# Kernel optimization log

Measured on AMD Instinct MI355X. Metric: run time of the kernel, lower is better.

## Reference

```python
import jax, jax.numpy as jnp
import numpy as np

B, S, D, H = 4, 4096, 2048, 512
EPS = 1e-5


def setup_inputs() -> dict:
    key = jax.random.key(0)
    ks = jax.random.split(key, 5)
    x = jax.random.normal(ks[0], (B, S, D), dtype=jnp.float32)
    ln_gamma = jnp.ones((D,), dtype=jnp.float32)
    ln_beta = jnp.zeros((D,), dtype=jnp.float32)
    # 'small' init: uniform in [1e-5 - 1e-6, 1e-5 + 1e-6]; use scaled randn here
    # so gradients are non-trivial, same math either way.
    W_down = jax.random.normal(ks[1], (H, D), dtype=jnp.float32) * 0.02
    b_down = jax.random.normal(ks[2], (H,), dtype=jnp.float32) * 0.02
    W_up = jax.random.normal(ks[3], (D, H), dtype=jnp.float32) * 0.02
    b_up = jax.random.normal(ks[4], (D,), dtype=jnp.float32) * 0.02
    return {"x": x, "ln_gamma": ln_gamma, "ln_beta": ln_beta,
            "W_down": W_down, "b_down": b_down, "W_up": W_up, "b_up": b_up}


def _layer_norm(x, gamma, beta):
    mu = jnp.mean(x, axis=-1, keepdims=True)
    var = jnp.mean(jnp.square(x - mu), axis=-1, keepdims=True)
    return (x - mu) * jax.lax.rsqrt(var + EPS) * gamma + beta


def reference(x, ln_gamma, ln_beta, W_down, b_down, W_up, b_up):
    # LayerNorm -> down-proj -> ReLU -> up-proj -> residual add
    y = _layer_norm(x, ln_gamma, ln_beta)                      # [B,S,D]
    y = jnp.einsum('bsd,hd->bsh', y, W_down) + b_down          # [B,S,H]
    y = jax.nn.relu(y)
    y = jnp.einsum('bsh,dh->bsd', y, W_up) + b_up              # [B,S,D]
    return x + y
```

## Files before the change

### kernel.cpp

```cpp
#include <hip/hip_runtime.h>

#define DD 2048
#define HH 512
#define NTOK 16384

typedef __attribute__((ext_vector_type(8))) short short8_t;
typedef __attribute__((ext_vector_type(4))) short short4_t;
typedef __attribute__((ext_vector_type(4))) float f32x4;

static __device__ __forceinline__ short f2bf(float f) {
    union { float f; unsigned u; } v; v.f = f;
    unsigned r = (v.u + 0x7fffu + ((v.u >> 16) & 1u)) >> 16;
    return (short)r;
}

static __device__ __forceinline__ void gl16(const short* g, short* l) {
    __builtin_amdgcn_global_load_lds(
        (const __attribute__((address_space(1))) unsigned int*)g,
        (__attribute__((address_space(3))) unsigned int*)l, 16, 0, 0);
}

__global__ __launch_bounds__(256) void k_wprep(
    const float* __restrict__ Wd, const float* __restrict__ g,
    const float* __restrict__ be, const float* __restrict__ Wu,
    short* __restrict__ Wg, short* __restrict__ Wub,
    float* __restrict__ c1, float* __restrict__ c2)
{
    int bid = blockIdx.x;
    if (bid < 128) {
        int w = threadIdx.x >> 6, lane = threadIdx.x & 63;
        int h = bid * 4 + w;
        const float* wr = Wd + (size_t)h * DD;
        float s1 = 0.f, s2 = 0.f;
        for (int i = 0; i < 8; i++) {
            int col = i * 256 + lane * 4;
            float4 wv = *(const float4*)(wr + col);
            float4 gv = *(const float4*)(g + col);
            float4 bv = *(const float4*)(be + col);
            s1 += gv.x * wv.x + gv.y * wv.y + gv.z * wv.z + gv.w * wv.w;
            s2 += bv.x * wv.x + bv.y * wv.y + bv.z * wv.z + bv.w * wv.w;
            short4_t o;
            o[0] = f2bf(wv.x * gv.x); o[1] = f2bf(wv.y * gv.y);
            o[2] = f2bf(wv.z * gv.z); o[3] = f2bf(wv.w * gv.w);
            *(short4_t*)(Wg + (size_t)h * DD + col) = o;
        }
        for (int m = 1; m < 64; m <<= 1) { s1 += __shfl_xor(s1, m); s2 += __shfl_xor(s2, m); }
        if (lane == 0) { c1[h] = s1; c2[h] = s2; }
    } else {
        int b = bid - 128;
        for (int r = 0; r < 4; r++) {
            int i = (b * 4 + r) * 1024 + threadIdx.x * 4;
            float4 v = *(const float4*)(Wu + i);
            short4_t o;
            o[0] = f2bf(v.x); o[1] = f2bf(v.y); o[2] = f2bf(v.z); o[3] = f2bf(v.w);
            *(short4_t*)(Wub + i) = o;
        }
    }
}

__global__ __launch_bounds__(256, 2) void k_down(
    const float* __restrict__ x, const short* __restrict__ Wg,
    const float* __restrict__ c1, const float* __restrict__ c2,
    const float* __restrict__ bd, short* __restrict__ hid)
{
    __shared__ __align__(16) short sA[2][128 * 64];
    __shared__ __align__(16) short sB[2][128 * 64];
    __shared__ float s_ps[128][8], s_pq[128][8];
    __shared__ float s_mu[128], s_rs[128];

    int bid = blockIdx.x;
    int nb = (bid & 7) * 64 + (bid >> 3);
    const int m0 = (nb >> 2) * 128;
    const int n0 = (nb & 3) * 128;

    const int tid = threadIdx.x, lane = tid & 63, w = tid >> 6;
    const int l15 = lane & 15, rg = lane >> 4;
    const int wm = w >> 1, wn = w & 1;
    const int sr = tid >> 3, sc = tid & 7;

    const float* xrow = x + (size_t)m0 * DD + (size_t)sr * DD + sc * 8;

    auto stageB = [&](int b, int kb) {
#pragma unroll
        for (int i = 0; i < 4; i++) {
            int ch = i * 256 + tid;
            int r = ch >> 3, c = ch & 7;
            gl16(Wg + (size_t)(n0 + r) * DD + kb + ((c ^ (r & 7)) << 3),
                 &sB[b][0] + (i * 256 + (w << 6)) * 8);
        }
    };

    float4 xv[4][2];
    auto loadA = [&](int kb) {
#pragma unroll
        for (int i = 0; i < 4; i++) {
            const float* p = xrow + (size_t)(i * 32) * DD + kb;
            xv[i][0] = *(const float4*)p;
            xv[i][1] = *(const float4*)(p + 4);
        }
    };
    float psum[4] = {0.f, 0.f, 0.f, 0.f}, psq[4] = {0.f, 0.f, 0.f, 0.f};
    auto writeA = [&](int b) {
#pragma unroll
        for (int i = 0; i < 4; i++) {
            float4 v0 = xv[i][0], v1 = xv[i][1];
            psum[i] += v0.x + v0.y + v0.z + v0.w + v1.x + v1.y + v1.z + v1.w;
            psq[i]  += v0.x * v0.x + v0.y * v0.y + v0.z * v0.z + v0.w * v0.w
                     + v1.x * v1.x + v1.y * v1.y + v1.z * v1.z + v1.w * v1.w;
            short8_t o;
            o[0] = f2bf(v0.x); o[1] = f2bf(v0.y); o[2] = f2bf(v0.z); o[3] = f2bf(v0.w);
            o[4] = f2bf(v1.x); o[5] = f2bf(v1.y); o[6] = f2bf(v1.z); o[7] = f2bf(v1.w);
            int r = i * 32 + sr;
            *(short8_t*)(&sA[b][0] + r * 64 + ((sc ^ (r & 7)) << 3)) = o;
        }
    };

    f32x4 acc[4][4];
#pragma unroll
    for (int i = 0; i < 4; i++)
#pragma unroll
        for (int j = 0; j < 4; j++) acc[i][j] = (f32x4){0.f, 0.f, 0.f, 0.f};

    stageB(0, 0);
    loadA(0);
    writeA(0);
    __syncthreads();

    for (int t = 0; t < 32; t++) {
        int cur = t & 1, nxt = cur ^ 1;
        if (t < 31) { stageB(nxt, (t + 1) * 64); loadA((t + 1) * 64); }
#pragma unroll
        for (int kk = 0; kk < 2; kk++) {
            int kc = kk * 4 + rg;
            short8_t af[4], bf[4];
#pragma unroll
            for (int mi = 0; mi < 4; mi++) {
                int rr = wm * 64 + mi * 16 + l15;
                af[mi] = *(const short8_t*)(&sA[cur][0] + rr * 64 + ((kc ^ (rr & 7)) << 3));
            }
#pragma unroll
            for (int ni = 0; ni < 4; ni++) {
                int rr = wn * 64 + ni * 16 + l15;
                bf[ni] = *(const short8_t*)(&sB[cur][0] + rr * 64 + ((kc ^ (rr & 7)) << 3));
            }
#pragma unroll
            for (int mi = 0; mi < 4; mi++)
#pragma unroll
                for (int ni = 0; ni < 4; ni++)
                    acc[mi][ni] = __builtin_amdgcn_mfma_f32_16x16x32_bf16(
                        af[mi], bf[ni], acc[mi][ni], 0, 0, 0);
        }
        if (t < 31) writeA(nxt);
        __syncthreads();
    }

#pragma unroll
    for (int i = 0; i < 4; i++) {
        s_ps[i * 32 + sr][sc] = psum[i];
        s_pq[i * 32 + sr][sc] = psq[i];
    }
    __syncthreads();
    if (tid < 128) {
        float s = 0.f, q = 0.f;
#pragma unroll
        for (int c = 0; c < 8; c++) { s += s_ps[tid][c]; q += s_pq[tid][c]; }
        float mu = s * (1.f / DD);
        float var = q * (1.f / DD) - mu * mu;
        s_mu[tid] = mu;
        s_rs[tid] = rsqrtf(var + 1e-5f);
    }
    __syncthreads();

#pragma unroll
    for (int ni = 0; ni < 4; ni++) {
        int h = n0 + wn * 64 + ni * 16 + l15;
        float C1 = c1[h];
        float C2 = c2[h] + bd[h];
#pragma unroll
        for (int mi = 0; mi < 4; mi++) {
#pragma unroll
            for (int j = 0; j < 4; j++) {
                int rowL = wm * 64 + mi * 16 + rg * 4 + j;
                float v = s_rs[rowL] * (acc[mi][ni][j] - s_mu[rowL] * C1) + C2;
                v = v > 0.f ? v : 0.f;
                hid[(size_t)(m0 + rowL) * HH + h] = f2bf(v);
            }
        }
    }
}

__global__ __launch_bounds__(256, 2) void k_up(
    const float* __restrict__ x, const short* __restrict__ hid,
    const short* __restrict__ Wub, const float* __restrict__ bu,
    float* __restrict__ out)
{
    __shared__ __align__(16) short sA[2][128 * 64];
    __shared__ __align__(16) short sB[2][128 * 64];

    int bid = blockIdx.x;
    int nb = (bid & 7) * 256 + (bid >> 3);
    const int m0 = (nb >> 4) * 128;
    const int n0 = (nb & 15) * 128;

    const int tid = threadIdx.x, lane = tid & 63, w = tid >> 6;
    const int l15 = lane & 15, rg = lane >> 4;
    const int wm = w >> 1, wn = w & 1;

    auto stage = [&](int b, int kb) {
#pragma unroll
        for (int i = 0; i < 4; i++) {
            int ch = i * 256 + tid;
            int r = ch >> 3, c = ch & 7;
            int co = ((c ^ (r & 7)) << 3);
            gl16(hid + (size_t)(m0 + r) * HH + kb + co,
                 &sA[b][0] + (i * 256 + (w << 6)) * 8);
            gl16(Wub + (size_t)(n0 + r) * HH + kb + co,
                 &sB[b][0] + (i * 256 + (w << 6)) * 8);
        }
    };

    f32x4 acc[4][4];
#pragma unroll
    for (int i = 0; i < 4; i++)
#pragma unroll
        for (int j = 0; j < 4; j++) acc[i][j] = (f32x4){0.f, 0.f, 0.f, 0.f};

    stage(0, 0);
    __syncthreads();

    for (int t = 0; t < 8; t++) {
        int cur = t & 1, nxt = cur ^ 1;
        if (t < 7) stage(nxt, (t + 1) * 64);
#pragma unroll
        for (int kk = 0; kk < 2; kk++) {
            int kc = kk * 4 + rg;
            short8_t af[4], bf[4];
#pragma unroll
            for (int mi = 0; mi < 4; mi++) {
                int rr = wm * 64 + mi * 16 + l15;
                af[mi] = *(const short8_t*)(&sA[cur][0] + rr * 64 + ((kc ^ (rr & 7)) << 3));
            }
#pragma unroll
            for (int ni = 0; ni < 4; ni++) {
                int rr = wn * 64 + ni * 16 + l15;
                bf[ni] = *(const short8_t*)(&sB[cur][0] + rr * 64 + ((kc ^ (rr & 7)) << 3));
            }
#pragma unroll
            for (int mi = 0; mi < 4; mi++)
#pragma unroll
                for (int ni = 0; ni < 4; ni++)
                    acc[mi][ni] = __builtin_amdgcn_mfma_f32_16x16x32_bf16(
                        af[mi], bf[ni], acc[mi][ni], 0, 0, 0);
        }
        __syncthreads();
    }

#pragma unroll
    for (int ni = 0; ni < 4; ni++) {
        int d = n0 + wn * 64 + ni * 16 + l15;
        float B = bu[d];
#pragma unroll
        for (int mi = 0; mi < 4; mi++) {
#pragma unroll
            for (int j = 0; j < 4; j++) {
                int rowL = wm * 64 + mi * 16 + rg * 4 + j;
                size_t idx = (size_t)(m0 + rowL) * DD + d;
                out[idx] = x[idx] + B + acc[mi][ni][j];
            }
        }
    }
}

extern "C" void kernel_launch(void* const* d_in, const int* in_sizes, int n_in,
                              void* d_out, int out_size, void* d_ws, size_t ws_size,
                              hipStream_t stream) {
    const float* x     = (const float*)d_in[0];
    const float* gamma = (const float*)d_in[1];
    const float* beta  = (const float*)d_in[2];
    const float* Wd_f  = (const float*)d_in[3];
    const float* bd    = (const float*)d_in[4];
    const float* Wu_f  = (const float*)d_in[5];
    const float* bu    = (const float*)d_in[6];

    short* Wg  = (short*)d_ws;
    short* Wub = Wg + (size_t)HH * DD;
    float* c1  = (float*)(Wub + (size_t)DD * HH);
    float* c2  = c1 + HH;
    short* hid = (short*)(c2 + HH);

    k_wprep<<<384, 256, 0, stream>>>(Wd_f, gamma, beta, Wu_f, Wg, Wub, c1, c2);
    k_down<<<(NTOK / 128) * (HH / 128), 256, 0, stream>>>(x, Wg, c1, c2, bd, hid);
    k_up<<<(NTOK / 128) * (DD / 128), 256, 0, stream>>>(x, hid, Wub, bu, (float*)d_out);
}
```

Before: 158.1 us.

## Precompute normalized bf16 activations in prep pass and simplify down-projection GEMM

Moves the LayerNorm statistics and normalization out of the down-projection kernel into a per-row prep pass that writes bf16 normalized activations to workspace. The down GEMM then stages both operands with async global-to-LDS loads and drops the in-loop fp32 conversion, the partial-sum bookkeeping and the mean-correction epilogue. In exchange it adds an extra full pass over x and a bf16 intermediate buffer write and read.

```diff
diff --git a/kernel.cpp b/kernel.cpp
--- a/kernel.cpp
+++ b/kernel.cpp
@@ -20,33 +20,34 @@
         (__attribute__((address_space(3))) unsigned int*)l, 16, 0, 0);
 }
 
-__global__ __launch_bounds__(256) void k_wprep(
+__global__ __launch_bounds__(256) void k_prep(
     const float* __restrict__ Wd, const float* __restrict__ g,
     const float* __restrict__ be, const float* __restrict__ Wu,
+    const float* __restrict__ x,
     short* __restrict__ Wg, short* __restrict__ Wub,
-    float* __restrict__ c1, float* __restrict__ c2)
+    float* __restrict__ c2, short* __restrict__ xn)
 {
+    __shared__ float ss[4], sq[4];
     int bid = blockIdx.x;
+    int w = threadIdx.x >> 6, lane = threadIdx.x & 63;
     if (bid < 128) {
-        int w = threadIdx.x >> 6, lane = threadIdx.x & 63;
         int h = bid * 4 + w;
         const float* wr = Wd + (size_t)h * DD;
-        float s1 = 0.f, s2 = 0.f;
+        float s2 = 0.f;
         for (int i = 0; i < 8; i++) {
             int col = i * 256 + lane * 4;
             float4 wv = *(const float4*)(wr + col);
             float4 gv = *(const float4*)(g + col);
             float4 bv = *(const float4*)(be + col);
-            s1 += gv.x * wv.x + gv.y * wv.y + gv.z * wv.z + gv.w * wv.w;
             s2 += bv.x * wv.x + bv.y * wv.y + bv.z * wv.z + bv.w * wv.w;
             short4_t o;
             o[0] = f2bf(wv.x * gv.x); o[1] = f2bf(wv.y * gv.y);
             o[2] = f2bf(wv.z * gv.z); o[3] = f2bf(wv.w * gv.w);
             *(short4_t*)(Wg + (size_t)h * DD + col) = o;
         }
-        for (int m = 1; m < 64; m <<= 1) { s1 += __shfl_xor(s1, m); s2 += __shfl_xor(s2, m); }
-        if (lane == 0) { c1[h] = s1; c2[h] = s2; }
-    } else {
+        for (int m = 1; m < 64; m <<= 1) s2 += __shfl_xor(s2, m);
+        if (lane == 0) c2[h] = s2;
+    } else if (bid < 384) {
         int b = bid - 128;
         for (int r = 0; r < 4; r++) {
             int i = (b * 4 + r) * 1024 + threadIdx.x * 4;
@@ -55,18 +56,37 @@
             o[0] = f2bf(v.x); o[1] = f2bf(v.y); o[2] = f2bf(v.z); o[3] = f2bf(v.w);
             *(short4_t*)(Wub + i) = o;
         }
+    } else {
+        int row = bid - 384;
+        const float* xr = x + (size_t)row * DD + threadIdx.x * 8;
+        float4 a = *(const float4*)xr;
+        float4 b = *(const float4*)(xr + 4);
+        float s = a.x + a.y + a.z + a.w + b.x + b.y + b.z + b.w;
+        float q = a.x * a.x + a.y * a.y + a.z * a.z + a.w * a.w
+                + b.x * b.x + b.y * b.y + b.z * b.z + b.w * b.w;
+        for (int m = 1; m < 64; m <<= 1) { s += __shfl_xor(s, m); q += __shfl_xor(q, m); }
+        if (lane == 0) { ss[w] = s; sq[w] = q; }
+        __syncthreads();
+        float S = ss[0] + ss[1] + ss[2] + ss[3];
+        float Q = sq[0] + sq[1] + sq[2] + sq[3];
+        float mu = S * (1.f / DD);
+        float rs = rsqrtf(Q * (1.f / DD) - mu * mu + 1e-5f);
+        short8_t o;
+        o[0] = f2bf((a.x - mu) * rs); o[1] = f2bf((a.y - mu) * rs);
+        o[2] = f2bf((a.z - mu) * rs); o[3] = f2bf((a.w - mu) * rs);
+        o[4] = f2bf((b.x - mu) * rs); o[5] = f2bf((b.y - mu) * rs);
+        o[6] = f2bf((b.z - mu) * rs); o[7] = f2bf((b.w - mu) * rs);
+        *(short8_t*)(xn + (size_t)row * DD + threadIdx.x * 8) = o;
     }
 }
 
 __global__ __launch_bounds__(256, 2) void k_down(
-    const float* __restrict__ x, const short* __restrict__ Wg,
-    const float* __restrict__ c1, const float* __restrict__ c2,
-    const float* __restrict__ bd, short* __restrict__ hid)
+    const short* __restrict__ xn, const short* __restrict__ Wg,
+    const float* __restrict__ c2, const float* __restrict__ bd,
+    short* __restrict__ hid)
 {
     __shared__ __align__(16) short sA[2][128 * 64];
     __shared__ __align__(16) short sB[2][128 * 64];
-    __shared__ float s_ps[128][8], s_pq[128][8];
-    __shared__ float s_mu[128], s_rs[128];
 
     int bid = blockIdx.x;
     int nb = (bid & 7) * 64 + (bid >> 3);
@@ -76,59 +96,32 @@
     const int tid = threadIdx.x, lane = tid & 63, w = tid >> 6;
     const int l15 = lane & 15, rg = lane >> 4;
     const int wm = w >> 1, wn = w & 1;
-    const int sr = tid >> 3, sc = tid & 7;
-
-    const float* xrow = x + (size_t)m0 * DD + (size_t)sr * DD + sc * 8;
-
-    auto stageB = [&](int b, int kb) {
+
+    auto stage = [&](int b, int kb) {
 #pragma unroll
         for (int i = 0; i < 4; i++) {
             int ch = i * 256 + tid;
             int r = ch >> 3, c = ch & 7;
-            gl16(Wg + (size_t)(n0 + r) * DD + kb + ((c ^ (r & 7)) << 3),
+            int co = ((c ^ (r & 7)) << 3);
+            gl16(xn + (size_t)(m0 + r) * DD + kb + co,
+                 &sA[b][0] + (i * 256 + (w << 6)) * 8);
+            gl16(Wg + (size_t)(n0 + r) * DD + kb + co,
                  &sB[b][0] + (i * 256 + (w << 6)) * 8);
         }
     };
 
-    float4 xv[4][2];
-    auto loadA = [&](int kb) {
-#pragma unroll
-        for (int i = 0; i < 4; i++) {
-            const float* p = xrow + (size_t)(i * 32) * DD + kb;
-            xv[i][0] = *(const float4*)p;
-            xv[i][1] = *(const float4*)(p + 4);
-        }
-    };
-    float psum[4] = {0.f, 0.f, 0.f, 0.f}, psq[4] = {0.f, 0.f, 0.f, 0.f};
-    auto writeA = [&](int b) {
-#pragma unroll
-        for (int i = 0; i < 4; i++) {
-            float4 v0 = xv[i][0], v1 = xv[i][1];
-            psum[i] += v0.x + v0.y + v0.z + v0.w + v1.x + v1.y + v1.z + v1.w;
-            psq[i]  += v0.x * v0.x + v0.y * v0.y + v0.z * v0.z + v0.w * v0.w
-                     + v1.x * v1.x + v1.y * v1.y + v1.z * v1.z + v1.w * v1.w;
-            short8_t o;
-            o[0] = f2bf(v0.x); o[1] = f2bf(v0.y); o[2] = f2bf(v0.z); o[3] = f2bf(v0.w);
-            o[4] = f2bf(v1.x); o[5] = f2bf(v1.y); o[6] = f2bf(v1.z); o[7] = f2bf(v1.w);
-            int r = i * 32 + sr;
-            *(short8_t*)(&sA[b][0] + r * 64 + ((sc ^ (r & 7)) << 3)) = o;
-        }
-    };
-
     f32x4 acc[4][4];
 #pragma unroll
     for (int i = 0; i < 4; i++)
 #pragma unroll
         for (int j = 0; j < 4; j++) acc[i][j] = (f32x4){0.f, 0.f, 0.f, 0.f};
 
-    stageB(0, 0);
-    loadA(0);
-    writeA(0);
+    stage(0, 0);
     __syncthreads();
 
     for (int t = 0; t < 32; t++) {
         int cur = t & 1, nxt = cur ^ 1;
-        if (t < 31) { stageB(nxt, (t + 1) * 64); loadA((t + 1) * 64); }
+        if (t < 31) stage(nxt, (t + 1) * 64);
 #pragma unroll
         for (int kk = 0; kk < 2; kk++) {
             int kc = kk * 4 + rg;
@@ -150,38 +143,19 @@
                     acc[mi][ni] = __builtin_amdgcn_mfma_f32_16x16x32_bf16(
                         af[mi], bf[ni], acc[mi][ni], 0, 0, 0);
         }
-        if (t < 31) writeA(nxt);
         __syncthreads();
     }
-
-#pragma unroll
-    for (int i = 0; i < 4; i++) {
-        s_ps[i * 32 + sr][sc] = psum[i];
-        s_pq[i * 32 + sr][sc] = psq[i];
-    }
-    __syncthreads();
-    if (tid < 128) {
-        float s = 0.f, q = 0.f;
-#pragma unroll
-        for (int c = 0; c < 8; c++) { s += s_ps[tid][c]; q += s_pq[tid][c]; }
-        float mu = s * (1.f / DD);
-        float var = q * (1.f / DD) - mu * mu;
-        s_mu[tid] = mu;
-        s_rs[tid] = rsqrtf(var + 1e-5f);
-    }
-    __syncthreads();
 
 #pragma unroll
     for (int ni = 0; ni < 4; ni++) {
         int h = n0 + wn * 64 + ni * 16 + l15;
-        float C1 = c1[h];
-        float C2 = c2[h] + bd[h];
+        float C = c2[h] + bd[h];
 #pragma unroll
         for (int mi = 0; mi < 4; mi++) {
 #pragma unroll
             for (int j = 0; j < 4; j++) {
                 int rowL = wm * 64 + mi * 16 + rg * 4 + j;
-                float v = s_rs[rowL] * (acc[mi][ni][j] - s_mu[rowL] * C1) + C2;
+                float v = acc[mi][ni][j] + C;
                 v = v > 0.f ? v : 0.f;
                 hid[(size_t)(m0 + rowL) * HH + h] = f2bf(v);
             }
@@ -284,11 +258,11 @@
 
     short* Wg  = (short*)d_ws;
     short* Wub = Wg + (size_t)HH * DD;
-    float* c1  = (float*)(Wub + (size_t)DD * HH);
-    float* c2  = c1 + HH;
+    float* c2  = (float*)(Wub + (size_t)DD * HH);
     short* hid = (short*)(c2 + HH);
-
-    k_wprep<<<384, 256, 0, stream>>>(Wd_f, gamma, beta, Wu_f, Wg, Wub, c1, c2);
-    k_down<<<(NTOK / 128) * (HH / 128), 256, 0, stream>>>(x, Wg, c1, c2, bd, hid);
+    short* xn  = hid + (size_t)NTOK * HH;
+
+    k_prep<<<384 + NTOK, 256, 0, stream>>>(Wd_f, gamma, beta, Wu_f, x, Wg, Wub, c2, xn);
+    k_down<<<(NTOK / 128) * (HH / 128), 256, 0, stream>>>(xn, Wg, c2, bd, hid);
     k_up<<<(NTOK / 128) * (DD / 128), 256, 0, stream>>>(x, hid, Wub, bu, (float*)d_out);
 }
```

Result: no change. 155.9 us (-1.4%).
